# Optimization experiments

Hardware: AMD Instinct MI355X
Metric: run time of the kernel (lower is better)

Reference implementation:

```python
import jax, jax.numpy as jnp
import numpy as np

N, E, M, G = 100000, 1600000, 20000, 512
IN, ED, OUT, H, C = 64, 16, 64, 4, 8


def segment_softmax(alpha, seg, num):
    # alpha: [Etot, H]; softmax over edges sharing the same destination segment
    amax = jax.ops.segment_max(alpha, seg, num_segments=num)
    amax = jnp.where(jnp.isneginf(amax), 0.0, amax)
    ex = jnp.exp(alpha - amax[seg])
    den = jax.ops.segment_sum(ex, seg, num_segments=num)
    return ex / (den[seg] + 1e-16)


def gat_conv(x, src, dst, ea, W, We, a_s, a_d, a_e, b, concat):
    # PyG GATConv: shared lin for src/dst, edge-conditioned attention, self loops pre-added
    n = x.shape[0]
    h, c = a_s.shape
    hx = (x @ W).reshape(n, h, c)            # [N,H,C]
    ee = (ea @ We).reshape(-1, h, c)          # [Etot,H,C]
    alpha = jax.nn.leaky_relu((hx * a_s).sum(-1)[src] + (hx * a_d).sum(-1)[dst] + (ee * a_e).sum(-1), 0.2)
    alpha = segment_softmax(alpha, dst, n)    # [Etot,H]
    out = jax.ops.segment_sum(hx[src] * alpha[:, :, None], dst, num_segments=n)
    out = out.reshape(n, h * c) if concat else out.mean(axis=1)
    return out + b


def setup_inputs() -> dict:
    keys = iter(jax.random.split(jax.random.key(0), 64))

    def nrm(shape, s=0.1):
        return jax.random.normal(next(keys), shape, jnp.float32) * s

    inp = {}
    inp["x"] = jax.random.normal(next(keys), (N, IN), jnp.float32)
    inp["edge_index"] = jax.random.randint(next(keys), (2, E), 0, N)
    inp["edge_attr"] = jax.random.normal(next(keys), (E, ED), jnp.float32)
    inp["scatter_index"] = jax.random.randint(next(keys), (N,), 0, M)
    inp["scatter_norm"] = jax.random.uniform(next(keys), (M, 1), jnp.float32, 0.5, 2.0)
    inp["nodes"] = jax.random.randint(next(keys), (M,), 0, G)
    inp["decision_var_indexes"] = jax.random.randint(next(keys), (G,), 0, N)
    dims = [(IN, H, C), (H * C, H, C), (H * C, H, C), (H * C, H, OUT)]
    for i, (din, hh, cc) in enumerate(dims, 1):
        inp[f"W{i}"] = nrm((din, hh * cc))
        inp[f"We{i}"] = nrm((ED, hh * cc))
        inp[f"asrc{i}"] = nrm((hh, cc))
        inp[f"adst{i}"] = nrm((hh, cc))
        inp[f"ae{i}"] = nrm((hh, cc))
        inp[f"b{i}"] = nrm((hh * cc if i < 4 else cc,))
    inp["Wp"] = nrm((OUT, OUT))
    inp["Wt"] = nrm((OUT, OUT))
    inp["Wo"] = nrm((2 * OUT, 1))
    inp["bo"] = nrm((1,))
    return inp


def reference(x, edge_index, edge_attr, scatter_index, scatter_norm, nodes, decision_var_indexes,
              W1, We1, asrc1, adst1, ae1, b1, W2, We2, asrc2, adst2, ae2, b2,
              W3, We3, asrc3, adst3, ae3, b3, W4, We4, asrc4, adst4, ae4, b4,
              Wp, Wt, Wo, bo):
    # add self loops once; edge_attr fill_value='mean' (PyG GATConv default)
    loop = jnp.arange(N)
    src = jnp.concatenate([edge_index[0], loop])
    dst = jnp.concatenate([edge_index[1], loop])
    ea = jnp.concatenate([edge_attr, jnp.broadcast_to(edge_attr.mean(0), (N, ED))], 0)
    lrelu = lambda v: jax.nn.leaky_relu(v, 0.01)
    h1 = lrelu(gat_conv(x, src, dst, ea, W1, We1, asrc1, adst1, ae1, b1, True))
    h2 = lrelu(gat_conv(h1, src, dst, ea, W2, We2, asrc2, adst2, ae2, b2, True))
    h3 = lrelu(gat_conv(h2, src, dst, ea, W3, We3, asrc3, adst3, ae3, b3, True))
    h4 = lrelu(gat_conv(h3, src, dst, ea, W4, We4, asrc4, adst4, ae4, b4, False))
    pool = jax.ops.segment_sum(h4, scatter_index, num_segments=M) / scatter_norm
    pool = jax.ops.segment_sum(pool, nodes, num_segments=G)   # [G,OUT]
    tgt = h4[decision_var_indexes]                             # [G,OUT]
    feat = lrelu(jnp.concatenate([pool @ Wp, tgt @ Wt], axis=1))
    return feat @ Wo + bo
```

## Files before the change

kernel.cpp:

```cpp
#include <hip/hip_runtime.h>
#include <math.h>

#define NN 100000
#define EE 1600000
#define ETOT 1700000
#define MM 20000
#define GG 512

#define NBUCK 782
#define NB1 256
#define CAP 4096

static constexpr int NB_N256 = (NN + 255) / 256;
static constexpr int NB_E256 = (ETOT + 255) / 256;
static constexpr int NB_AGG  = NN / 32;

#define SM_MEAN 0
#define SM_WEA 16
#define SM_VS4 272
#define SM_VD4 400
#define SM_W4P 536
#define SM_TOTAL 8728

typedef unsigned long long ull;

__device__ __forceinline__ unsigned short f2bf(float f) {
  unsigned int u = __float_as_uint(f);
  u += 0x7fffu + ((u >> 16) & 1u);
  return (unsigned short)(u >> 16);
}
__device__ __forceinline__ float bf2f(unsigned int h) {
  return __uint_as_float(h << 16);
}
__device__ __forceinline__ float lrelu(float v, float s) { return v > 0.f ? v : s * v; }

__global__ __launch_bounds__(256) void k_pre(
    float* __restrict__ sm, const float* __restrict__ We1, const float* __restrict__ We2,
    const float* __restrict__ We3, const float* __restrict__ We4,
    const float* __restrict__ ae1, const float* __restrict__ ae2,
    const float* __restrict__ ae3, const float* __restrict__ ae4,
    const float* __restrict__ as4, const float* __restrict__ ad4,
    const float* __restrict__ W4) {
  int t = threadIdx.x;
  {
    int l = t >> 6, d = (t >> 2) & 15, h = t & 3;
    const float* We = (l == 0) ? We1 : (l == 1) ? We2 : (l == 2) ? We3 : We4;
    const float* ae = (l == 0) ? ae1 : (l == 1) ? ae2 : (l == 2) ? ae3 : ae4;
    int C = (l == 3) ? 64 : 8;
    float s = 0.f;
    for (int c = 0; c < C; c++) s += We[d * (4 * C) + h * C + c] * ae[h * C + c];
    sm[SM_WEA + l * 64 + d * 4 + h] = s;
  }
  if (t < 128) {
    int k = t >> 2, h = t & 3;
    float s1 = 0.f, s2 = 0.f;
    for (int c = 0; c < 64; c++) {
      float w = W4[k * 256 + h * 64 + c];
      s1 += w * as4[h * 64 + c];
      s2 += w * ad4[h * 64 + c];
    }
    sm[SM_VS4 + t] = s1;
    sm[SM_VD4 + t] = s2;
  }
  for (int i = t; i < 8192; i += 256) {
    int row = i >> 6, c = i & 63;
    int h = row >> 5, k = row & 31;
    sm[SM_W4P + i] = 0.25f * W4[k * 256 + h * 64 + c];
  }
}

__global__ __launch_bounds__(1024) void k_hist1(const int* __restrict__ ei,
                                                const float* __restrict__ ea,
                                                int* __restrict__ blk_cnt,
                                                float* __restrict__ sm) {
  __shared__ int hist[NBUCK];
  __shared__ float lsum[16];
  int t = threadIdx.x;
  for (int i = t; i < NBUCK; i += 1024) hist[i] = 0;
  if (t < 16) lsum[t] = 0.f;
  __syncthreads();
  for (int e = blockIdx.x * 1024 + t; e < ETOT; e += NB1 * 1024) {
    int dst = (e < EE) ? ei[EE + e] : (e - EE);
    atomicAdd(&hist[dst >> 7], 1);
  }
  {
    const float4* ea4 = (const float4*)ea;
    int q = t & 3;
    float4 a = make_float4(0.f, 0.f, 0.f, 0.f);
    for (size_t i = (size_t)blockIdx.x * 1024 + t; i < (size_t)EE * 4;
         i += (size_t)NB1 * 1024) {
      float4 v = ea4[i];
      a.x += v.x; a.y += v.y; a.z += v.z; a.w += v.w;
    }
    for (int m = 4; m < 64; m <<= 1) {
      a.x += __shfl_xor(a.x, m, 64);
      a.y += __shfl_xor(a.y, m, 64);
      a.z += __shfl_xor(a.z, m, 64);
      a.w += __shfl_xor(a.w, m, 64);
    }
    if ((t & 63) < 4) {
      atomicAdd(&lsum[q * 4 + 0], a.x);
      atomicAdd(&lsum[q * 4 + 1], a.y);
      atomicAdd(&lsum[q * 4 + 2], a.z);
      atomicAdd(&lsum[q * 4 + 3], a.w);
    }
  }
  __syncthreads();
  for (int i = t; i < NBUCK; i += 1024) blk_cnt[blockIdx.x * NBUCK + i] = hist[i];
  if (t < 16) atomicAdd(&sm[SM_MEAN + t], lsum[t]);
}

__global__ __launch_bounds__(256) void k_bscan_a(const int* __restrict__ blk_cnt,
                                                 int* __restrict__ blk_base_T,
                                                 int* __restrict__ bucket_tot) {
  __shared__ int s[256];
  int b = blockIdx.x, t = threadIdx.x;
  int v = blk_cnt[t * NBUCK + b];
  s[t] = v;
  __syncthreads();
  for (int off = 1; off < 256; off <<= 1) {
    int x = (t >= off) ? s[t - off] : 0;
    __syncthreads();
    s[t] += x;
    __syncthreads();
  }
  blk_base_T[b * 256 + t] = s[t] - v;
  if (t == 255) bucket_tot[b] = s[255];
}

__global__ __launch_bounds__(1024) void k_bscan_b(const int* __restrict__ bucket_tot,
                                                  int* __restrict__ bucket_base,
                                                  int* __restrict__ row_off) {
  __shared__ int s[1024];
  int t = threadIdx.x;
  int v = (t < NBUCK) ? bucket_tot[t] : 0;
  s[t] = v;
  __syncthreads();
  for (int off = 1; off < 1024; off <<= 1) {
    int x = (t >= off) ? s[t - off] : 0;
    __syncthreads();
    s[t] += x;
    __syncthreads();
  }
  if (t < NBUCK) bucket_base[t] = s[t] - v;
  if (t == 0) {
    bucket_base[NBUCK] = ETOT;
    row_off[NN] = ETOT;
  }
}

__global__ __launch_bounds__(1024) void k_scatter1(const int* __restrict__ ei,
                                                   const int* __restrict__ bucket_base,
                                                   const int* __restrict__ blk_base_T,
                                                   uint2* __restrict__ pairs) {
  __shared__ int base[NBUCK];
  __shared__ int rank[NBUCK];
  int t = threadIdx.x, blk = blockIdx.x;
  for (int i = t; i < NBUCK; i += 1024) {
    base[i] = bucket_base[i] + blk_base_T[i * 256 + blk];
    rank[i] = 0;
  }
  __syncthreads();
  for (int e = blk * 1024 + t; e < ETOT; e += NB1 * 1024) {
    int src, dst;
    if (e < EE) {
      src = ei[e];
      dst = ei[EE + e];
    } else {
      src = dst = e - EE;
    }
    int bin = dst >> 7;
    int r = atomicAdd(&rank[bin], 1);
    pairs[base[bin] + r] =
        make_uint2((unsigned)src, (unsigned)e | ((unsigned)(dst & 127) << 21));
  }
}

__global__ __launch_bounds__(256) void k_sort2(const uint2* __restrict__ pairs,
                                               const int* __restrict__ bucket_base,
                                               int* __restrict__ row_off,
                                               int* __restrict__ csr_src,
                                               int* __restrict__ eidx) {
  __shared__ uint2 plds[CAP];
  __shared__ unsigned short perm[CAP];
  __shared__ int hist[128];
  __shared__ int scan[128];
  __shared__ int rankv[128];
  int b = blockIdx.x, t = threadIdx.x;
  int start = bucket_base[b], end = bucket_base[b + 1];
  int cnt = end - start;
  if (t < 128) hist[t] = 0;
  __syncthreads();
  bool fits = (cnt <= CAP);
  if (fits) {
    for (int i = t; i < cnt; i += 256) {
      uint2 pe = pairs[start + i];
      plds[i] = pe;
      atomicAdd(&hist[(pe.y >> 21) & 127], 1);
    }
  } else {
    for (int i = t; i < cnt; i += 256)
      atomicAdd(&hist[(pairs[start + i].y >> 21) & 127], 1);
  }
  __syncthreads();
  if (t < 128) scan[t] = hist[t];
  __syncthreads();
  for (int off = 1; off < 128; off <<= 1) {
    int x = (t >= off && t < 128) ? scan[t - off] : 0;
    __syncthreads();
    if (t < 128) scan[t] += x;
    __syncthreads();
  }
  if (t < 128) {
    int excl = scan[t] - hist[t];
    rankv[t] = excl;
    int dst = b * 128 + t;
    if (dst < NN) row_off[dst] = start + excl;
  }
  __syncthreads();
  if (fits) {
    for (int i = t; i < cnt; i += 256) {
      int bin = (plds[i].y >> 21) & 127;
      int r = atomicAdd(&rankv[bin], 1);
      perm[r] = (unsigned short)i;
    }
    __syncthreads();
    for (int r = t; r < cnt; r += 256) {
      uint2 pe = plds[perm[r]];
      csr_src[start + r] = (int)pe.x;
      eidx[start + r] = (int)(pe.y & 0x1fffffu);
    }
  } else {
    for (int i = t; i < cnt; i += 256) {
      uint2 pe = pairs[start + i];
      int bin = (pe.y >> 21) & 127;
      int r = atomicAdd(&rankv[bin], 1);
      csr_src[start + r] = (int)pe.x;
      eidx[start + r] = (int)(pe.y & 0x1fffffu);
    }
  }
}

__global__ __launch_bounds__(256) void k_pack(const int* __restrict__ eidx,
                                              const float* __restrict__ ea,
                                              const float* __restrict__ sm,
                                              ull* __restrict__ apc) {
  __shared__ float sWea[256];
  __shared__ float smean[16];
  int t = threadIdx.x;
  sWea[t] = sm[SM_WEA + t];
  if (t < 16) smean[t] = sm[SM_MEAN + t] * (1.f / EE);
  __syncthreads();
  int pos = blockIdx.x * 256 + t;
  if (pos >= ETOT) return;
  int eid = eidx[pos];
  float eav[16];
  if (eid < EE) {
    const float4* p = (const float4*)(ea + (size_t)eid * 16);
    float4 v0 = p[0], v1 = p[1], v2 = p[2], v3 = p[3];
    eav[0] = v0.x; eav[1] = v0.y; eav[2] = v0.z; eav[3] = v0.w;
    eav[4] = v1.x; eav[5] = v1.y; eav[6] = v1.z; eav[7] = v1.w;
    eav[8] = v2.x; eav[9] = v2.y; eav[10] = v2.z; eav[11] = v2.w;
    eav[12] = v3.x; eav[13] = v3.y; eav[14] = v3.z; eav[15] = v3.w;
  } else {
#pragma unroll
    for (int d = 0; d < 16; d++) eav[d] = smean[d];
  }
#pragma unroll
  for (int l = 0; l < 4; l++) {
    ull pk = 0;
#pragma unroll
    for (int h = 0; h < 4; h++) {
      float s = 0.f;
#pragma unroll
      for (int d = 0; d < 16; d++) s += eav[d] * sWea[l * 64 + d * 4 + h];
      pk |= (ull)f2bf(s) << (16 * h);
    }
    apc[(size_t)l * ETOT + pos] = pk;
  }
}

template <int DIN>
__global__ __launch_bounds__(256) void k_t(const float* __restrict__ in,
                                           const float* __restrict__ W,
                                           const float* __restrict__ a_s,
                                           const float* __restrict__ a_d,
                                           unsigned short* __restrict__ hxb,
                                           float* __restrict__ ssrc,
                                           float* __restrict__ sdst) {
  __shared__ float4 sW[DIN * 8];
  __shared__ float sas[32], sad[32];
  int t = threadIdx.x;
  for (int i = t; i < DIN * 8; i += 256) sW[i] = ((const float4*)W)[i];
  if (t < 32) { sas[t] = a_s[t]; sad[t] = a_d[t]; }
  __syncthreads();
  int n = blockIdx.x * 256 + t;
  if (n >= NN) return;
  float acc[32];
#pragma unroll
  for (int j = 0; j < 32; j++) acc[j] = 0.f;
  const float* xr = in + (size_t)n * DIN;
  for (int k = 0; k < DIN; k += 4) {
    float4 xv = *(const float4*)(xr + k);
    float xa[4] = {xv.x, xv.y, xv.z, xv.w};
#pragma unroll
    for (int kk = 0; kk < 4; kk++) {
#pragma unroll
      for (int j4 = 0; j4 < 8; j4++) {
        float4 ww = sW[(k + kk) * 8 + j4];
        acc[j4 * 4 + 0] += xa[kk] * ww.x;
        acc[j4 * 4 + 1] += xa[kk] * ww.y;
        acc[j4 * 4 + 2] += xa[kk] * ww.z;
        acc[j4 * 4 + 3] += xa[kk] * ww.w;
      }
    }
  }
  float ssum[4], dsum[4];
#pragma unroll
  for (int h = 0; h < 4; h++) {
    float s = 0.f, d = 0.f;
#pragma unroll
    for (int c = 0; c < 8; c++) {
      s += acc[h * 8 + c] * sas[h * 8 + c];
      d += acc[h * 8 + c] * sad[h * 8 + c];
    }
    ssum[h] = s;
    dsum[h] = d;
  }
  unsigned int up[16];
#pragma unroll
  for (int i = 0; i < 16; i++)
    up[i] = (unsigned)f2bf(acc[2 * i]) | ((unsigned)f2bf(acc[2 * i + 1]) << 16);
  uint4* ho = (uint4*)(hxb + (size_t)n * 32);
  ho[0] = make_uint4(up[0], up[1], up[2], up[3]);
  ho[1] = make_uint4(up[4], up[5], up[6], up[7]);
  ho[2] = make_uint4(up[8], up[9], up[10], up[11]);
  ho[3] = make_uint4(up[12], up[13], up[14], up[15]);
  ((float4*)ssrc)[n] = make_float4(ssum[0], ssum[1], ssum[2], ssum[3]);
  ((float4*)sdst)[n] = make_float4(dsum[0], dsum[1], dsum[2], dsum[3]);
}

__global__ __launch_bounds__(256) void k_t4(const float* __restrict__ h3,
                                            const float* __restrict__ sm,
                                            unsigned short* __restrict__ h3b,
                                            float* __restrict__ ssrc,
                                            float* __restrict__ sdst) {
  __shared__ float sVs[128], sVd[128];
  int t = threadIdx.x;
  if (t < 128) { sVs[t] = sm[SM_VS4 + t]; sVd[t] = sm[SM_VD4 + t]; }
  __syncthreads();
  int n = blockIdx.x * 256 + t;
  if (n >= NN) return;
  const float* r = h3 + (size_t)n * 32;
  float v[32];
#pragma unroll
  for (int k = 0; k < 32; k++) v[k] = r[k];
  float s0 = 0, s1 = 0, s2 = 0, s3 = 0, d0 = 0, d1 = 0, d2 = 0, d3 = 0;
#pragma unroll
  for (int k = 0; k < 32; k++) {
    s0 += v[k] * sVs[k * 4 + 0]; s1 += v[k] * sVs[k * 4 + 1];
    s2 += v[k] * sVs[k * 4 + 2]; s3 += v[k] * sVs[k * 4 + 3];
    d0 += v[k] * sVd[k * 4 + 0]; d1 += v[k] * sVd[k * 4 + 1];
    d2 += v[k] * sVd[k * 4 + 2]; d3 += v[k] * sVd[k * 4 + 3];
  }
  unsigned int up[16];
#pragma unroll
  for (int i = 0; i < 16; i++)
    up[i] = (unsigned)f2bf(v[2 * i]) | ((unsigned)f2bf(v[2 * i + 1]) << 16);
  uint4* ho = (uint4*)(h3b + (size_t)n * 32);
  ho[0] = make_uint4(up[0], up[1], up[2], up[3]);
  ho[1] = make_uint4(up[4], up[5], up[6], up[7]);
  ho[2] = make_uint4(up[8], up[9], up[10], up[11]);
  ho[3] = make_uint4(up[12], up[13], up[14], up[15]);
  ((float4*)ssrc)[n] = make_float4(s0, s1, s2, s3);
  ((float4*)sdst)[n] = make_float4(d0, d1, d2, d3);
}

__global__ __launch_bounds__(256) void k_agg(const int* __restrict__ row_off,
                                             const int* __restrict__ csr_src,
                                             const ull* __restrict__ apl,
                                             const unsigned short* __restrict__ hxb,
                                             const float* __restrict__ ssrc,
                                             const float* __restrict__ sdst,
                                             const float* __restrict__ bias,
                                             float* __restrict__ outp) {
  int t = threadIdx.x;
  int g = t >> 3, j = t & 7, h = j >> 1;
  int n = blockIdx.x * 32 + g;
  if (n >= NN) return;
  float sd = sdst[n * 4 + h];
  int e0 = row_off[n], e1 = row_off[n + 1];
  float den = 0.f;
  float4 acc = make_float4(0.f, 0.f, 0.f, 0.f);
  for (int e = e0; e < e1; ++e) {
    int src = csr_src[e];
    ull pk = apl[e];
    float ae = bf2f((unsigned int)(unsigned short)(pk >> (16 * h)));
    float al = ssrc[src * 4 + h] + sd + ae;
    al = fminf(lrelu(al, 0.2f), 80.f);
    uint2 u = *(const uint2*)(hxb + (size_t)src * 32 + (j << 2));
    float p = __expf(al);
    den += p;
    acc.x += p * bf2f(u.x & 0xffffu);
    acc.y += p * bf2f(u.x >> 16);
    acc.z += p * bf2f(u.y & 0xffffu);
    acc.w += p * bf2f(u.y >> 16);
  }
  float inv = 1.f / (den + 1e-16f);
  float4 b = *(const float4*)(bias + (j << 2));
  float4 o;
  o.x = lrelu(acc.x * inv + b.x, 0.01f);
  o.y = lrelu(acc.y * inv + b.y, 0.01f);
  o.z = lrelu(acc.z * inv + b.z, 0.01f);
  o.w = lrelu(acc.w * inv + b.w, 0.01f);
  *(float4*)(outp + (size_t)n * 32 + (j << 2)) = o;
}

__global__ __launch_bounds__(256) void k_agg4(const int* __restrict__ row_off,
                                              const int* __restrict__ csr_src,
                                              const ull* __restrict__ apl,
                                              const unsigned short* __restrict__ h3b,
                                              const float* __restrict__ ssrc,
                                              const float* __restrict__ sdst,
                                              unsigned short* __restrict__ aggb) {
  int t = threadIdx.x;
  int g = t >> 3, j = t & 7;
  int n = blockIdx.x * 32 + g;
  if (n >= NN) return;
  float4 sdv = ((const float4*)sdst)[n];
  float sda[4] = {sdv.x, sdv.y, sdv.z, sdv.w};
  int e0 = row_off[n], e1 = row_off[n + 1];
  float den[4];
  float4 acc[4];
#pragma unroll
  for (int h = 0; h < 4; h++) {
    den[h] = 0.f;
    acc[h] = make_float4(0.f, 0.f, 0.f, 0.f);
  }
  for (int e = e0; e < e1; ++e) {
    int src = csr_src[e];
    ull pk = apl[e];
    float4 ssv = ((const float4*)ssrc)[src];
    float ssa[4] = {ssv.x, ssv.y, ssv.z, ssv.w};
    uint2 u = *(const uint2*)(h3b + (size_t)src * 32 + (j << 2));
    float hx0 = bf2f(u.x & 0xffffu), hx1 = bf2f(u.x >> 16);
    float hx2 = bf2f(u.y & 0xffffu), hx3 = bf2f(u.y >> 16);
#pragma unroll
    for (int h = 0; h < 4; h++) {
      float al = ssa[h] + sda[h] + bf2f((unsigned int)(unsigned short)(pk >> (16 * h)));
      al = fminf(lrelu(al, 0.2f), 80.f);
      float p = __expf(al);
      den[h] += p;
      acc[h].x += p * hx0;
      acc[h].y += p * hx1;
      acc[h].z += p * hx2;
      acc[h].w += p * hx3;
    }
  }
#pragma unroll
  for (int h = 0; h < 4; h++) {
    float inv = 1.f / (den[h] + 1e-16f);
    unsigned int u0 = (unsigned)f2bf(acc[h].x * inv) | ((unsigned)f2bf(acc[h].y * inv) << 16);
    unsigned int u1 = (unsigned)f2bf(acc[h].z * inv) | ((unsigned)f2bf(acc[h].w * inv) << 16);
    *(uint2*)(aggb + (size_t)n * 128 + h * 32 + (j << 2)) = make_uint2(u0, u1);
  }
}

__global__ __launch_bounds__(256) void k_epi4(const unsigned short* __restrict__ aggb,
                                              const float* __restrict__ sm,
                                              const float* __restrict__ b4,
                                              float* __restrict__ h4) {
  __shared__ float4 sW[2048];
  __shared__ float sb[64];
  int t = threadIdx.x;
  for (int i = t; i < 2048; i += 256) sW[i] = ((const float4*)(sm + SM_W4P))[i];
  if (t < 64) sb[t] = b4[t];
  __syncthreads();
  int n = blockIdx.x * 256 + t;
  if (n >= NN) return;
  float acc[64];
#pragma unroll
  for (int j = 0; j < 64; j++) acc[j] = 0.f;
  const unsigned short* r = aggb + (size_t)n * 128;
  for (int k = 0; k < 128; k += 4) {
    uint2 u = *(const uint2*)(r + k);
    float va[4] = {bf2f(u.x & 0xffffu), bf2f(u.x >> 16), bf2f(u.y & 0xffffu),
                   bf2f(u.y >> 16)};
#pragma unroll
    for (int kk = 0; kk < 4; kk++) {
#pragma unroll
      for (int j4 = 0; j4 < 16; j4++) {
        float4 wv = sW[(k + kk) * 16 + j4];
        acc[j4 * 4 + 0] += va[kk] * wv.x;
        acc[j4 * 4 + 1] += va[kk] * wv.y;
        acc[j4 * 4 + 2] += va[kk] * wv.z;
        acc[j4 * 4 + 3] += va[kk] * wv.w;
      }
    }
  }
  float* o = h4 + (size_t)n * 64;
#pragma unroll
  for (int j4 = 0; j4 < 16; j4++) {
    float4 ov;
    ov.x = lrelu(acc[j4 * 4 + 0] + sb[j4 * 4 + 0], 0.01f);
    ov.y = lrelu(acc[j4 * 4 + 1] + sb[j4 * 4 + 1], 0.01f);
    ov.z = lrelu(acc[j4 * 4 + 2] + sb[j4 * 4 + 2], 0.01f);
    ov.w = lrelu(acc[j4 * 4 + 3] + sb[j4 * 4 + 3], 0.01f);
    ((float4*)o)[j4] = ov;
  }
}

__global__ __launch_bounds__(256) void k_pool1(const float* __restrict__ h4,
                                               const int* __restrict__ sidx,
                                               float* __restrict__ pool1) {
  int i = blockIdx.x * 256 + threadIdx.x;
  if (i >= NN * 64) return;
  int n = i >> 6, c = i & 63;
  atomicAdd(&pool1[(size_t)sidx[n] * 64 + c], h4[i]);
}

__global__ __launch_bounds__(256) void k_pool2(const float* __restrict__ pool1,
                                               const float* __restrict__ snorm,
                                               const int* __restrict__ nodes,
                                               float* __restrict__ pool2) {
  int i = blockIdx.x * 256 + threadIdx.x;
  if (i >= MM * 64) return;
  int mi = i >> 6, c = i & 63;
  float v = pool1[i] / snorm[mi];
  atomicAdd(&pool2[(size_t)nodes[mi] * 64 + c], v);
}

__global__ __launch_bounds__(64) void k_final(const float* __restrict__ pool2,
                                              const float* __restrict__ h4,
                                              const int* __restrict__ dvi,
                                              const float* __restrict__ Wp,
                                              const float* __restrict__ Wt,
                                              const float* __restrict__ Wo,
                                              const float* __restrict__ bo,
                                              float* __restrict__ out) {
  __shared__ float p[64], tt[64];
  int gI = blockIdx.x, j = threadIdx.x;
  p[j] = pool2[gI * 64 + j];
  tt[j] = h4[(size_t)dvi[gI] * 64 + j];
  __syncthreads();
  float f1 = 0.f, f2 = 0.f;
#pragma unroll 8
  for (int c = 0; c < 64; c++) {
    f1 += p[c] * Wp[c * 64 + j];
    f2 += tt[c] * Wt[c * 64 + j];
  }
  f1 = lrelu(f1, 0.01f);
  f2 = lrelu(f2, 0.01f);
  float v = f1 * Wo[j] + f2 * Wo[64 + j];
  for (int off = 32; off > 0; off >>= 1) v += __shfl_down(v, off, 64);
  if (j == 0) out[gI] = v + bo[0];
}

extern "C" void kernel_launch(void* const* d_in, const int* in_sizes, int n_in,
                              void* d_out, int out_size, void* d_ws, size_t ws_size,
                              hipStream_t stream) {
  const float* x = (const float*)d_in[0];
  const int* ei = (const int*)d_in[1];
  const float* ea = (const float*)d_in[2];
  const int* sidx = (const int*)d_in[3];
  const float* snorm = (const float*)d_in[4];
  const int* nodes = (const int*)d_in[5];
  const int* dvi = (const int*)d_in[6];
  const float* W1 = (const float*)d_in[7];
  const float* as1 = (const float*)d_in[9];
  const float* ad1 = (const float*)d_in[10];
  const float* b1 = (const float*)d_in[12];
  const float* W2 = (const float*)d_in[13];
  const float* as2 = (const float*)d_in[15];
  const float* ad2 = (const float*)d_in[16];
  const float* b2 = (const float*)d_in[18];
  const float* W3 = (const float*)d_in[19];
  const float* as3 = (const float*)d_in[21];
  const float* ad3 = (const float*)d_in[22];
  const float* b3 = (const float*)d_in[24];
  const float* b4 = (const float*)d_in[30];
  const float* Wp = (const float*)d_in[31];
  const float* Wt = (const float*)d_in[32];
  const float* Wo = (const float*)d_in[33];
  const float* bo = (const float*)d_in[34];
  float* out = (float*)d_out;

  char* w = (char*)d_ws;
  size_t off = 0;
  auto take = [&](size_t bytes) -> char* {
    char* p = w + off;
    off = (off + bytes + 255) & ~(size_t)255;
    return p;
  };
  int* row_off = (int*)take((size_t)(NN + 1) * 4);
  float* sm = (float*)take(SM_TOTAL * 4);
  uint2* pairs = (uint2*)take((size_t)ETOT * 8);
  int* csr_src = (int*)take((size_t)ETOT * 4);
  int* eidx = (int*)take((size_t)ETOT * 4);
  ull* apc = (ull*)take((size_t)ETOT * 4 * 8);
  int* blk_cnt = (int*)take((size_t)NB1 * NBUCK * 4);
  int* blk_base_T = (int*)take((size_t)NBUCK * NB1 * 4);
  int* bucket_tot = (int*)take((size_t)NBUCK * 4);
  int* bucket_base = (int*)take((size_t)(NBUCK + 1) * 4);
  float* h4 = (float*)take((size_t)NN * 64 * 4);
  unsigned short* aggb = (unsigned short*)take((size_t)NN * 128 * 2);
  unsigned short* hxb = (unsigned short*)take((size_t)NN * 32 * 2);
  unsigned short* h3b = (unsigned short*)take((size_t)NN * 32 * 2);
  float* ssrc = (float*)take((size_t)NN * 4 * 4);
  float* sdst = (float*)take((size_t)NN * 4 * 4);
  float* bufA = (float*)take((size_t)NN * 32 * 4);
  float* bufB = (float*)take((size_t)NN * 32 * 4);
  float* pool1 = (float*)take((size_t)MM * 64 * 4);
  float* pool2 = (float*)take((size_t)GG * 64 * 4);
  if (off > ws_size) return;

  hipMemsetAsync(sm, 0, 64, stream);
  hipMemsetAsync(pool1, 0, (size_t)MM * 64 * 4, stream);
  hipMemsetAsync(pool2, 0, (size_t)GG * 64 * 4, stream);

  k_pre<<<1, 256, 0, stream>>>(sm, (const float*)d_in[8], (const float*)d_in[14],
                               (const float*)d_in[20], (const float*)d_in[26],
                               (const float*)d_in[11], (const float*)d_in[17],
                               (const float*)d_in[23], (const float*)d_in[29],
                               (const float*)d_in[27], (const float*)d_in[28],
                               (const float*)d_in[25]);

  k_hist1<<<NB1, 1024, 0, stream>>>(ei, ea, blk_cnt, sm);
  k_bscan_a<<<NBUCK, 256, 0, stream>>>(blk_cnt, blk_base_T, bucket_tot);
  k_bscan_b<<<1, 1024, 0, stream>>>(bucket_tot, bucket_base, row_off);
  k_scatter1<<<NB1, 1024, 0, stream>>>(ei, bucket_base, blk_base_T, pairs);
  k_sort2<<<NBUCK, 256, 0, stream>>>(pairs, bucket_base, row_off, csr_src, eidx);
  k_pack<<<NB_E256, 256, 0, stream>>>(eidx, ea, sm, apc);

  k_t<64><<<NB_N256, 256, 0, stream>>>(x, W1, as1, ad1, hxb, ssrc, sdst);
  k_agg<<<NB_AGG, 256, 0, stream>>>(row_off, csr_src, apc, hxb, ssrc, sdst, b1, bufA);
  k_t<32><<<NB_N256, 256, 0, stream>>>(bufA, W2, as2, ad2, hxb, ssrc, sdst);
  k_agg<<<NB_AGG, 256, 0, stream>>>(row_off, csr_src, apc + (size_t)ETOT, hxb, ssrc,
                                    sdst, b2, bufB);
  k_t<32><<<NB_N256, 256, 0, stream>>>(bufB, W3, as3, ad3, hxb, ssrc, sdst);
  k_agg<<<NB_AGG, 256, 0, stream>>>(row_off, csr_src, apc + 2 * (size_t)ETOT, hxb, ssrc,
                                    sdst, b3, bufA);
  k_t4<<<NB_N256, 256, 0, stream>>>(bufA, sm, h3b, ssrc, sdst);
  k_agg4<<<NB_AGG, 256, 0, stream>>>(row_off, csr_src, apc + 3 * (size_t)ETOT, h3b, ssrc,
                                     sdst, aggb);
  k_epi4<<<NB_N256, 256, 0, stream>>>(aggb, sm, b4, h4);

  k_pool1<<<(NN * 64) / 256, 256, 0, stream>>>(h4, sidx, pool1);
  k_pool2<<<(MM * 64) / 256, 256, 0, stream>>>(pool1, snorm, nodes, pool2);
  k_final<<<GG, 64, 0, stream>>>(pool2, h4, dvi, Wp, Wt, Wo, bo, out);
}
```

Baseline: 703.2 us.

## Process destination nodes in degree-sorted order in aggregation kernels

Adds a counting sort of nodes by in-degree (histogram, scan, permutation kernels) and has the four aggregation kernels process nodes through this permutation. Nodes with equal degree then share a wavefront, which reduces divergence from lanes waiting on the longest edge loop. The cost is three extra small kernel launches plus a memset, and output writes and row_off/sdst reads that are no longer contiguous in node order.

```diff
diff --git a/kernel.cpp b/kernel.cpp
--- a/kernel.cpp
+++ b/kernel.cpp
@@ -10,10 +10,12 @@
 #define NBUCK 782
 #define NB1 256
 #define CAP 4096
+#define DBINS 1024
 
 static constexpr int NB_N256 = (NN + 255) / 256;
 static constexpr int NB_E256 = (ETOT + 255) / 256;
 static constexpr int NB_AGG  = NN / 32;
+static constexpr int NB_N1024 = (NN + 1023) / 1024;
 
 #define SM_MEAN 0
 #define SM_WEA 16
@@ -241,6 +243,47 @@
   }
 }
 
+__global__ __launch_bounds__(1024) void k_dhist(const int* __restrict__ row_off,
+                                                int* __restrict__ dhist) {
+  __shared__ int h[DBINS];
+  int t = threadIdx.x;
+  h[t] = 0;
+  __syncthreads();
+  int n = blockIdx.x * 1024 + t;
+  if (n < NN) {
+    int deg = row_off[n + 1] - row_off[n];
+    atomicAdd(&h[deg & (DBINS - 1)], 1);
+  }
+  __syncthreads();
+  if (h[t]) atomicAdd(&dhist[t], h[t]);
+}
+
+__global__ __launch_bounds__(1024) void k_dscan(const int* __restrict__ dhist,
+                                                int* __restrict__ dcur) {
+  __shared__ int s[DBINS];
+  int t = threadIdx.x;
+  int v = dhist[t];
+  s[t] = v;
+  __syncthreads();
+  for (int off = 1; off < DBINS; off <<= 1) {
+    int x = (t >= off) ? s[t - off] : 0;
+    __syncthreads();
+    s[t] += x;
+    __syncthreads();
+  }
+  dcur[t] = s[t] - v;
+}
+
+__global__ __launch_bounds__(1024) void k_dperm(const int* __restrict__ row_off,
+                                                int* __restrict__ dcur,
+                                                int* __restrict__ dperm) {
+  int n = blockIdx.x * 1024 + threadIdx.x;
+  if (n >= NN) return;
+  int deg = row_off[n + 1] - row_off[n];
+  int pos = atomicAdd(&dcur[deg & (DBINS - 1)], 1);
+  dperm[pos] = n;
+}
+
 __global__ __launch_bounds__(256) void k_pack(const int* __restrict__ eidx,
                                               const float* __restrict__ ea,
                                               const float* __restrict__ sm,
@@ -376,7 +419,8 @@
   ((float4*)sdst)[n] = make_float4(d0, d1, d2, d3);
 }
 
-__global__ __launch_bounds__(256) void k_agg(const int* __restrict__ row_off,
+__global__ __launch_bounds__(256) void k_agg(const int* __restrict__ dperm,
+                                             const int* __restrict__ row_off,
                                              const int* __restrict__ csr_src,
                                              const ull* __restrict__ apl,
                                              const unsigned short* __restrict__ hxb,
@@ -386,8 +430,9 @@
                                              float* __restrict__ outp) {
   int t = threadIdx.x;
   int g = t >> 3, j = t & 7, h = j >> 1;
-  int n = blockIdx.x * 32 + g;
-  if (n >= NN) return;
+  int gid = blockIdx.x * 32 + g;
+  if (gid >= NN) return;
+  int n = dperm[gid];
   float sd = sdst[n * 4 + h];
   int e0 = row_off[n], e1 = row_off[n + 1];
   float den = 0.f;
@@ -416,7 +461,8 @@
   *(float4*)(outp + (size_t)n * 32 + (j << 2)) = o;
 }
 
-__global__ __launch_bounds__(256) void k_agg4(const int* __restrict__ row_off,
+__global__ __launch_bounds__(256) void k_agg4(const int* __restrict__ dperm,
+                                              const int* __restrict__ row_off,
                                               const int* __restrict__ csr_src,
                                               const ull* __restrict__ apl,
                                               const unsigned short* __restrict__ h3b,
@@ -425,8 +471,9 @@
                                               unsigned short* __restrict__ aggb) {
   int t = threadIdx.x;
   int g = t >> 3, j = t & 7;
-  int n = blockIdx.x * 32 + g;
-  if (n >= NN) return;
+  int gid = blockIdx.x * 32 + g;
+  if (gid >= NN) return;
+  int n = dperm[gid];
   float4 sdv = ((const float4*)sdst)[n];
   float sda[4] = {sdv.x, sdv.y, sdv.z, sdv.w};
   int e0 = row_off[n], e1 = row_off[n + 1];
@@ -602,6 +649,9 @@
   int* blk_base_T = (int*)take((size_t)NBUCK * NB1 * 4);
   int* bucket_tot = (int*)take((size_t)NBUCK * 4);
   int* bucket_base = (int*)take((size_t)(NBUCK + 1) * 4);
+  int* dhist = (int*)take((size_t)DBINS * 4);
+  int* dcur = (int*)take((size_t)DBINS * 4);
+  int* dperm = (int*)take((size_t)NN * 4);
   float* h4 = (float*)take((size_t)NN * 64 * 4);
   unsigned short* aggb = (unsigned short*)take((size_t)NN * 128 * 2);
   unsigned short* hxb = (unsigned short*)take((size_t)NN * 32 * 2);
@@ -615,6 +665,7 @@
   if (off > ws_size) return;
 
   hipMemsetAsync(sm, 0, 64, stream);
+  hipMemsetAsync(dhist, 0, (size_t)DBINS * 4, stream);
   hipMemsetAsync(pool1, 0, (size_t)MM * 64 * 4, stream);
   hipMemsetAsync(pool2, 0, (size_t)GG * 64 * 4, stream);
 
@@ -630,19 +681,23 @@
   k_bscan_b<<<1, 1024, 0, stream>>>(bucket_tot, bucket_base, row_off);
   k_scatter1<<<NB1, 1024, 0, stream>>>(ei, bucket_base, blk_base_T, pairs);
   k_sort2<<<NBUCK, 256, 0, stream>>>(pairs, bucket_base, row_off, csr_src, eidx);
+  k_dhist<<<NB_N1024, 1024, 0, stream>>>(row_off, dhist);
+  k_dscan<<<1, 1024, 0, stream>>>(dhist, dcur);
+  k_dperm<<<NB_N1024, 1024, 0, stream>>>(row_off, dcur, dperm);
   k_pack<<<NB_E256, 256, 0, stream>>>(eidx, ea, sm, apc);
 
   k_t<64><<<NB_N256, 256, 0, stream>>>(x, W1, as1, ad1, hxb, ssrc, sdst);
-  k_agg<<<NB_AGG, 256, 0, stream>>>(row_off, csr_src, apc, hxb, ssrc, sdst, b1, bufA);
+  k_agg<<<NB_AGG, 256, 0, stream>>>(dperm, row_off, csr_src, apc, hxb, ssrc, sdst, b1,
+                                    bufA);
   k_t<32><<<NB_N256, 256, 0, stream>>>(bufA, W2, as2, ad2, hxb, ssrc, sdst);
-  k_agg<<<NB_AGG, 256, 0, stream>>>(row_off, csr_src, apc + (size_t)ETOT, hxb, ssrc,
-                                    sdst, b2, bufB);
+  k_agg<<<NB_AGG, 256, 0, stream>>>(dperm, row_off, csr_src, apc + (size_t)ETOT, hxb,
+                                    ssrc, sdst, b2, bufB);
   k_t<32><<<NB_N256, 256, 0, stream>>>(bufB, W3, as3, ad3, hxb, ssrc, sdst);
-  k_agg<<<NB_AGG, 256, 0, stream>>>(row_off, csr_src, apc + 2 * (size_t)ETOT, hxb, ssrc,
-                                    sdst, b3, bufA);
+  k_agg<<<NB_AGG, 256, 0, stream>>>(dperm, row_off, csr_src, apc + 2 * (size_t)ETOT, hxb,
+                                    ssrc, sdst, b3, bufA);
   k_t4<<<NB_N256, 256, 0, stream>>>(bufA, sm, h3b, ssrc, sdst);
-  k_agg4<<<NB_AGG, 256, 0, stream>>>(row_off, csr_src, apc + 3 * (size_t)ETOT, h3b, ssrc,
-                                     sdst, aggb);
+  k_agg4<<<NB_AGG, 256, 0, stream>>>(dperm, row_off, csr_src, apc + 3 * (size_t)ETOT,
+                                     h3b, ssrc, sdst, aggb);
   k_epi4<<<NB_N256, 256, 0, stream>>>(aggb, sm, b4, h4);
 
   k_pool1<<<(NN * 64) / 256, 256, 0, stream>>>(h4, sidx, pool1);
```

Result: slower. 1.024 ms (+45.6%).
